# Performance work log

Measured on AMD Instinct MI355X. Metric: run time of the kernel, lower is better.

The kernel has to match this reference:

```python
import jax, jax.numpy as jnp
import numpy as np

N_NODES = 50000
N_EDGES = 800000
N_FEATS = 64
K_HOPS = 3


def setup_inputs() -> dict:
    key = jax.random.key(0)
    k1, k2, k3 = jax.random.split(key, 3)
    x = jax.random.normal(k1, (N_NODES, N_FEATS), dtype=jnp.float32)
    edge_index = jax.random.randint(k2, (2, N_EDGES), 0, N_NODES, dtype=jnp.int32)
    # SGConv linear: out_channels = 1 (hardcoded in Net)
    W = jax.random.normal(k3, (1, N_FEATS), dtype=jnp.float32) / np.sqrt(N_FEATS)
    b = jnp.zeros((1,), dtype=jnp.float32)
    return {"x": x, "edge_index": edge_index, "W": W, "b": b}


def reference(x, edge_index, W, b):
    # SGConv: X' = (D^-1/2 (A + I) D^-1/2)^K X @ W.T + b
    N = x.shape[0]
    self_loops = jnp.arange(N, dtype=edge_index.dtype)
    row = jnp.concatenate([edge_index[0], self_loops])  # source nodes (x_j)
    col = jnp.concatenate([edge_index[1], self_loops])  # destination nodes
    # gcn_norm: degree computed at destination with unit edge weights
    deg = jax.ops.segment_sum(jnp.ones(row.shape[0], x.dtype), col, num_segments=N)
    dinv = jnp.where(deg > 0, jax.lax.rsqrt(deg), jnp.zeros_like(deg))
    norm = dinv[row] * dinv[col]  # [E + N]
    # K hops of normalized sparse propagation: out[col] += norm * x[row]
    for _ in range(K_HOPS):
        x = jax.ops.segment_sum(norm[:, None] * x[row], col, num_segments=N)
    return x @ W.T + b  # [N, 1]
```

## Files before the change

### kernel.cpp

```cpp
#include <hip/hip_runtime.h>
#include <hip/hip_bf16.h>

#define N_NODES 50000
#define N_EDGES 800000
#define N_FEATS 64
#define EB4     (N_EDGES / 4)
#define NBUCK   256
#define BRANGE  196
#define CAPB    4096
#define BZT     1024


__global__ void k_zero_i(int* __restrict__ p, int n) {
    int i = blockIdx.x * blockDim.x + threadIdx.x;
    if (i < n) p[i] = 0;
}

__global__ void __launch_bounds__(BZT) k_bucketize(
    const int* __restrict__ row, const int* __restrict__ col,
    int* __restrict__ gcur, unsigned* __restrict__ recs)
{
    __shared__ int s_cnt[NBUCK];
    __shared__ int s_base[NBUCK];
    const int t = threadIdx.x;
    if (t < NBUCK) s_cnt[t] = 0;
    __syncthreads();

    const int g = blockIdx.x * BZT + t;
    const bool valid = g < EB4;
    int4 c4, r4;
    int bk[4], rk[4];
    if (valid) {
        c4 = ((const int4*)col)[g];
        r4 = ((const int4*)row)[g];
        bk[0] = c4.x / BRANGE; rk[0] = atomicAdd(&s_cnt[bk[0]], 1);
        bk[1] = c4.y / BRANGE; rk[1] = atomicAdd(&s_cnt[bk[1]], 1);
        bk[2] = c4.z / BRANGE; rk[2] = atomicAdd(&s_cnt[bk[2]], 1);
        bk[3] = c4.w / BRANGE; rk[3] = atomicAdd(&s_cnt[bk[3]], 1);
    }
    __syncthreads();
    if (t < NBUCK) {
        int n = s_cnt[t];
        s_base[t] = n ? atomicAdd(&gcur[t], n) : 0;
    }
    __syncthreads();
    if (valid) {
        int cc[4] = {c4.x, c4.y, c4.z, c4.w};
        int rr[4] = {r4.x, r4.y, r4.z, r4.w};
        #pragma unroll
        for (int i = 0; i < 4; i++) {
            int slot = s_base[bk[i]] + rk[i];
            unsigned rec = ((unsigned)(cc[i] - bk[i] * BRANGE) << 16) | (unsigned)rr[i];
            if (slot < CAPB) recs[(size_t)bk[i] * CAPB + slot] = rec;
        }
    }
}

__global__ void __launch_bounds__(512) k_prep(
    const int* __restrict__ gcur, const unsigned* __restrict__ recs,
    const float* __restrict__ x, const float* __restrict__ w,
    float* __restrict__ dinv, float* __restrict__ z0)
{
    __shared__ int   s_cnt[BRANGE];
    __shared__ float s_dinv[BRANGE];
    const int t = threadIdx.x;
    const int blk = blockIdx.x;
    const int own0 = blk * BRANGE;
    if (t < BRANGE) s_cnt[t] = 0;
    __syncthreads();

    const int sz  = min(gcur[blk], CAPB);
    const int sz2 = sz >> 1;
    const uint2* rb2 = (const uint2*)(recs + (size_t)blk * CAPB);
    for (int e = t; e < sz2; e += 512) {
        uint2 r = rb2[e];
        atomicAdd(&s_cnt[r.x >> 16], 1);
        atomicAdd(&s_cnt[r.y >> 16], 1);
    }
    if (t == 0 && (sz & 1)) {
        unsigned r = recs[(size_t)blk * CAPB + sz - 1];
        atomicAdd(&s_cnt[r >> 16], 1);
    }
    __syncthreads();

    if (t < BRANGE) {
        float d = rsqrtf((float)(s_cnt[t] + 1));
        s_dinv[t] = d;
        int node = own0 + t;
        if (node < N_NODES) dinv[node] = d;
    }
    __syncthreads();

    if (t < BRANGE) {
        int node = own0 + t;
        if (node < N_NODES) {
            const float4* xr = (const float4*)(x + (size_t)node * N_FEATS);
            const float4* wr = (const float4*)w;
            float acc = 0.0f;
            #pragma unroll
            for (int k = 0; k < N_FEATS / 4; k++) {
                float4 v = xr[k];
                float4 u = wr[k];
                acc += v.x * u.x + v.y * u.y + v.z * u.z + v.w * u.w;
            }
            z0[node] = s_dinv[t] * acc;
        }
    }
}

template <bool FINAL>
__global__ void __launch_bounds__(512) k_hop(
    const int* __restrict__ gcur, const unsigned* __restrict__ recs,
    const float* __restrict__ dinv, const float* __restrict__ zin,
    float* __restrict__ out, const float* __restrict__ bptr)
{
    __shared__ float acc[BRANGE];
    const int t = threadIdx.x;
    const int blk = blockIdx.x;
    if (t < BRANGE) acc[t] = 0.0f;
    __syncthreads();
    const int sz  = min(gcur[blk], CAPB);
    const int sz2 = sz >> 1;
    const uint2* rb2 = (const uint2*)(recs + (size_t)blk * CAPB);
    for (int e = t; e < sz2; e += 512) {
        uint2 r = rb2[e];
        atomicAdd(&acc[r.x >> 16], zin[r.x & 0xFFFFu]);
        atomicAdd(&acc[r.y >> 16], zin[r.y & 0xFFFFu]);
    }
    if (t == 0 && (sz & 1)) {
        unsigned r = recs[(size_t)blk * CAPB + sz - 1];
        atomicAdd(&acc[r >> 16], zin[r & 0xFFFFu]);
    }
    __syncthreads();
    if (t < BRANGE) {
        int node = blk * BRANGE + t;
        if (node < N_NODES) {
            float d = dinv[node];
            float v = zin[node] + acc[t];
            out[node] = FINAL ? (d * v + bptr[0]) : (d * d * v);
        }
    }
}


extern "C" void kernel_launch(void* const* d_in, const int* in_sizes, int n_in,
                              void* d_out, int out_size, void* d_ws, size_t ws_size,
                              hipStream_t stream) {
    const float* x  = (const float*)d_in[0];
    const int*   ei = (const int*)d_in[1];
    const float* W  = (const float*)d_in[2];
    const float* b  = (const float*)d_in[3];
    float* out = (float*)d_out;

    const int* row = ei;
    const int* col = ei + N_EDGES;

    int*      gcur = (int*)d_ws;
    unsigned* recs = (unsigned*)(gcur + NBUCK);
    float*    dinv = (float*)(recs + (size_t)NBUCK * CAPB);
    float*    z0   = dinv + N_NODES;
    float*    z1   = z0 + N_NODES;

    k_zero_i<<<1, NBUCK, 0, stream>>>(gcur, NBUCK);
    k_bucketize<<<(EB4 + BZT - 1) / BZT, BZT, 0, stream>>>(row, col, gcur, recs);
    k_prep<<<NBUCK, 512, 0, stream>>>(gcur, recs, x, W, dinv, z0);

    k_hop<false><<<NBUCK, 512, 0, stream>>>(gcur, recs, dinv, z0, z1, nullptr);
    k_hop<false><<<NBUCK, 512, 0, stream>>>(gcur, recs, dinv, z1, z0, nullptr);
    k_hop<true ><<<NBUCK, 512, 0, stream>>>(gcur, recs, dinv, z0, out, b);
}
```

Baseline: 102.0 us.

## Move x·W projection into bucketize kernel and replace zero kernel with memset

The per-node dot product of x with W now runs inside the bucketize kernel across its ~196 blocks of 1024 threads and writes an intermediate vector u. The prep kernel then only computes dinv and scales u, so it no longer streams all of x with only 196 threads per block over 256 blocks. The small zeroing kernel is replaced by hipMemsetAsync. This costs an extra N-float write and read of u, and the bucketize blocks do more work.

```diff
diff --git a/kernel.cpp b/kernel.cpp
--- a/kernel.cpp
+++ b/kernel.cpp
@@ -11,14 +11,10 @@
 #define BZT     1024
 
 
-__global__ void k_zero_i(int* __restrict__ p, int n) {
-    int i = blockIdx.x * blockDim.x + threadIdx.x;
-    if (i < n) p[i] = 0;
-}
-
 __global__ void __launch_bounds__(BZT) k_bucketize(
     const int* __restrict__ row, const int* __restrict__ col,
-    int* __restrict__ gcur, unsigned* __restrict__ recs)
+    const float* __restrict__ x, const float* __restrict__ w,
+    int* __restrict__ gcur, unsigned* __restrict__ recs, float* __restrict__ u)
 {
     __shared__ int s_cnt[NBUCK];
     __shared__ int s_base[NBUCK];
@@ -54,15 +50,26 @@
             if (slot < CAPB) recs[(size_t)bk[i] * CAPB + slot] = rec;
         }
     }
+
+    if (g < N_NODES) {
+        const float4* xr = (const float4*)(x + (size_t)g * N_FEATS);
+        const float4* wr = (const float4*)w;
+        float acc = 0.0f;
+        #pragma unroll
+        for (int k = 0; k < N_FEATS / 4; k++) {
+            float4 v = xr[k];
+            float4 q = wr[k];
+            acc += v.x * q.x + v.y * q.y + v.z * q.z + v.w * q.w;
+        }
+        u[g] = acc;
+    }
 }
 
 __global__ void __launch_bounds__(512) k_prep(
     const int* __restrict__ gcur, const unsigned* __restrict__ recs,
-    const float* __restrict__ x, const float* __restrict__ w,
-    float* __restrict__ dinv, float* __restrict__ z0)
+    const float* __restrict__ u, float* __restrict__ dinv, float* __restrict__ z0)
 {
-    __shared__ int   s_cnt[BRANGE];
-    __shared__ float s_dinv[BRANGE];
+    __shared__ int s_cnt[BRANGE];
     const int t = threadIdx.x;
     const int blk = blockIdx.x;
     const int own0 = blk * BRANGE;
@@ -84,26 +91,11 @@
     __syncthreads();
 
     if (t < BRANGE) {
-        float d = rsqrtf((float)(s_cnt[t] + 1));
-        s_dinv[t] = d;
-        int node = own0 + t;
-        if (node < N_NODES) dinv[node] = d;
-    }
-    __syncthreads();
-
-    if (t < BRANGE) {
         int node = own0 + t;
         if (node < N_NODES) {
-            const float4* xr = (const float4*)(x + (size_t)node * N_FEATS);
-            const float4* wr = (const float4*)w;
-            float acc = 0.0f;
-            #pragma unroll
-            for (int k = 0; k < N_FEATS / 4; k++) {
-                float4 v = xr[k];
-                float4 u = wr[k];
-                acc += v.x * u.x + v.y * u.y + v.z * u.z + v.w * u.w;
-            }
-            z0[node] = s_dinv[t] * acc;
+            float d = rsqrtf((float)(s_cnt[t] + 1));
+            dinv[node] = d;
+            z0[node] = d * u[node];
         }
     }
 }
@@ -158,12 +150,14 @@
     int*      gcur = (int*)d_ws;
     unsigned* recs = (unsigned*)(gcur + NBUCK);
     float*    dinv = (float*)(recs + (size_t)NBUCK * CAPB);
-    float*    z0   = dinv + N_NODES;
+    float*    u    = dinv + N_NODES;
+    float*    z0   = u + N_NODES;
     float*    z1   = z0 + N_NODES;
 
-    k_zero_i<<<1, NBUCK, 0, stream>>>(gcur, NBUCK);
-    k_bucketize<<<(EB4 + BZT - 1) / BZT, BZT, 0, stream>>>(row, col, gcur, recs);
-    k_prep<<<NBUCK, 512, 0, stream>>>(gcur, recs, x, W, dinv, z0);
+    hipMemsetAsync(gcur, 0, NBUCK * sizeof(int), stream);
+
+    k_bucketize<<<(EB4 + BZT - 1) / BZT, BZT, 0, stream>>>(row, col, x, W, gcur, recs, u);
+    k_prep<<<NBUCK, 512, 0, stream>>>(gcur, recs, u, dinv, z0);
 
     k_hop<false><<<NBUCK, 512, 0, stream>>>(gcur, recs, dinv, z0, z1, nullptr);
     k_hop<false><<<NBUCK, 512, 0, stream>>>(gcur, recs, dinv, z1, z0, nullptr);
```

Result: slower. 108.2 us (+6.0%).
